# Kernel tuning notes

Hardware: AMD Instinct MI355X
Metric: run time of the kernel (lower is better)

## Reference

```python
import jax, jax.numpy as jnp
import numpy as np

N_NODES = 100000
NUM_LAYER = 3
REG_WEIGHT = 1e-4


def setup_inputs() -> dict:
    key = jax.random.key(0)
    ks = jax.random.split(key, 6)
    E = 1280000
    B = 4096
    D = 64
    # xavier-uniform-like scale for embedding table
    emb_weight = jax.random.normal(ks[0], (N_NODES, D), dtype=jnp.float32) * 0.01
    src = jax.random.randint(ks[1], (E,), 0, N_NODES, dtype=jnp.int32)
    dst = jax.random.randint(ks[2], (E,), 0, N_NODES, dtype=jnp.int32)
    users = jax.random.randint(ks[3], (B,), 0, N_NODES, dtype=jnp.int32)
    pos = jax.random.randint(ks[4], (B,), 0, N_NODES, dtype=jnp.int32)
    neg = jax.random.randint(ks[5], (B,), 0, N_NODES, dtype=jnp.int32)
    return {"emb_weight": emb_weight, "src": src, "dst": dst,
            "users": users, "pos": pos, "neg": neg}


def _edge_norm(src, dst):
    # DGL norm(): d = sum of edge mask (ones) per dst node; adj_e = d[src]^-0.5 * d[dst]^-0.5
    ones = jnp.ones(src.shape[0], dtype=jnp.float32)
    deg = jax.ops.segment_sum(ones, dst, num_segments=N_NODES)
    dinv = jnp.where(deg > 0, deg ** -0.5, 0.0)  # inf -> 0 handling
    return dinv[src] * dinv[dst]  # [E]


def _propagate(emb_weight, src, dst, adj):
    # LightGCN propagation: h_{l+1}[v] = sum_{(u->v)} adj_e * h_l[u]
    h = emb_weight
    layers = [h]
    for _ in range(NUM_LAYER):
        m = h[src] * adj[:, None]                    # [E, D] gather + edge weight
        h = jax.ops.segment_sum(m, dst, num_segments=N_NODES)  # [N, D] scatter-sum
        layers.append(h)
    return jnp.mean(jnp.stack(layers, axis=1), axis=1)  # mean over L+1 layers


def reference(emb_weight, src, dst, users, pos, neg):
    adj = _edge_norm(src, dst)
    all_emb = _propagate(emb_weight, src, dst, adj)

    u_e, p_e, n_e = all_emb[users], all_emb[pos], all_emb[neg]
    u0, p0, n0 = emb_weight[users], emb_weight[pos], emb_weight[neg]

    B = users.shape[0]
    reg_loss = 0.5 * (jnp.sum(u0 ** 2) + jnp.sum(p0 ** 2) + jnp.sum(n0 ** 2)) / B
    reg_loss = reg_loss * REG_WEIGHT

    pos_scores = jnp.sum(u_e * p_e, axis=1)
    neg_scores = jnp.sum(u_e * n_e, axis=1)
    loss_emb = jnp.mean(jax.nn.softplus(neg_scores - pos_scores))

    loss = loss_emb + reg_loss
    return loss, loss_emb, reg_loss
```

## Files before the change

### kernel.cpp

```cpp
#include <hip/hip_runtime.h>
#include <hip/hip_fp8.h>
#include <math.h>

#define N_NODES 100000
#define DIM 64
#define NUM_LAYER 3
#define BATCH 4096
#define REG_WEIGHT 1e-4f
#define NBUCKET 391
#define STAGE_CAP 4096
#define CURPAD 16
#define H_SCALE 64.0f
#define H_INV_SCALE (1.0f / 64.0f)

typedef float floatx2 __attribute__((ext_vector_type(2)));

__device__ unsigned char g_hf8[2][(size_t)N_NODES * DIM];
__device__ float g_sums[(size_t)3 * BATCH * DIM];
__device__ int   g_row_ptr[N_NODES + 1];
__device__ float g_dinv[N_NODES];
__device__ int   g_bcur[NBUCKET * CURPAD];
__device__ unsigned int g_stage[NBUCKET * STAGE_CAP];
__device__ int   g_csr[1280000];
__device__ int2  g_csr2[1280000];
__device__ int   g_shead[N_NODES];
__device__ int   g_snext[3 * BATCH];
__device__ float g_part_sp[BATCH];
__device__ float g_part_rg[BATCH];

__device__ inline void fma4_fp8(unsigned int d, float w,
                                float& a0, float& a1, float& a2, float& a3) {
    floatx2 lo = __builtin_amdgcn_cvt_pk_f32_fp8((int)d, false);
    floatx2 hi = __builtin_amdgcn_cvt_pk_f32_fp8((int)d, true);
    a0 = fmaf(w, lo.x, a0); a1 = fmaf(w, lo.y, a1);
    a2 = fmaf(w, hi.x, a2); a3 = fmaf(w, hi.y, a3);
}
__device__ inline unsigned int pack4_fp8(float a0, float a1, float a2, float a3) {
    int w = __builtin_amdgcn_cvt_pk_fp8_f32(a0, a1, 0, false);
    w     = __builtin_amdgcn_cvt_pk_fp8_f32(a2, a3, w, true);
    return (unsigned int)w;
}

#define EDGES_PER_THREAD 8
__global__ void __launch_bounds__(1024) stage_buckets(const int* __restrict__ src,
                                                      const int* __restrict__ dst, int E,
                                                      const int* __restrict__ users,
                                                      const int* __restrict__ pos,
                                                      const int* __restrict__ neg,
                                                      const float* __restrict__ emb) {
    __shared__ int h[NBUCKET];
    __shared__ int cur[NBUCKET];
    int tid = threadIdx.x;
    int gt = blockIdx.x * 1024 + tid;
    if (gt < 3 * BATCH) {
        int which = gt / BATCH, s = gt - which * BATCH;
        const int* idx = (which == 0) ? users : ((which == 1) ? pos : neg);
        g_snext[gt] = atomicExch(&g_shead[idx[s]], gt + 1);
    }
    int base = blockIdx.x * (1024 * EDGES_PER_THREAD);
    for (int i = tid; i < NBUCKET; i += 1024) h[i] = 0;
    __syncthreads();
    int myd[EDGES_PER_THREAD], mys[EDGES_PER_THREAD];
    #pragma unroll
    for (int k = 0; k < EDGES_PER_THREAD; ++k) {
        int e = base + k * 1024 + tid;
        if (e < E) {
            myd[k] = dst[e]; mys[k] = src[e];
            atomicAdd(&h[myd[k] >> 8], 1);
        } else myd[k] = -1;
    }
    __syncthreads();
    for (int i = tid; i < NBUCKET; i += 1024) {
        int c = h[i];
        cur[i] = c ? (atomicAdd(&g_bcur[i * CURPAD], c) + i * STAGE_CAP) : 0;
    }
    __syncthreads();
    #pragma unroll
    for (int k = 0; k < EDGES_PER_THREAD; ++k) {
        if (myd[k] >= 0) {
            int p = atomicAdd(&cur[myd[k] >> 8], 1);
            g_stage[p] = (unsigned int)((mys[k] << 8) | (myd[k] & 255));
        }
    }
    {
        const int NW = N_NODES * DIM / 4;
        int stride = gridDim.x * 1024;
        unsigned int* hw = (unsigned int*)g_hf8[0];
        for (int k = blockIdx.x * 1024 + tid; k < NW; k += stride) {
            const float* e = emb + (size_t)k * 4;
            hw[k] = pack4_fp8(e[0] * H_SCALE, e[1] * H_SCALE,
                              e[2] * H_SCALE, e[3] * H_SCALE);
        }
    }
}

__global__ void __launch_bounds__(512) finalize_place() {
    __shared__ int cs[512];
    __shared__ int lh[256], sc[256], cur[256];
    int b = blockIdx.x, t = threadIdx.x;
    int c = (t < NBUCKET) ? g_bcur[t * CURPAD] : 0;
    cs[t] = c;
    __syncthreads();
    for (int off = 1; off < 512; off <<= 1) {
        int x = (t >= off) ? cs[t - off] : 0;
        __syncthreads();
        cs[t] += x;
        __syncthreads();
    }
    int mybase = (b > 0) ? cs[b - 1] : 0;
    int cnt    = cs[b] - mybase;
    if (b == 0 && t == 0) g_row_ptr[N_NODES] = cs[NBUCKET - 1];
    int sbeg = b * STAGE_CAP;
    if (t < 256) lh[t] = 0;
    __syncthreads();
    for (int k = t; k < cnt; k += 512)
        atomicAdd(&lh[g_stage[sbeg + k] & 255], 1);
    __syncthreads();
    int v = 0;
    if (t < 256) { v = lh[t]; sc[t] = v; }
    __syncthreads();
    for (int off = 1; off < 256; off <<= 1) {
        int x = (t >= off && t < 256) ? sc[t - off] : 0;
        __syncthreads();
        if (t < 256) sc[t] += x;
        __syncthreads();
    }
    if (t < 256) {
        int start = mybase + sc[t] - v;
        cur[t] = start;
        int node = (b << 8) + t;
        if (node < N_NODES) {
            g_row_ptr[node] = start;
            g_dinv[node]    = (v > 0) ? rsqrtf((float)v) : 0.0f;
        }
    }
    __syncthreads();
    for (int k = t; k < cnt; k += 512) {
        unsigned int e = g_stage[sbeg + k];
        int pos = atomicAdd(&cur[e & 255], 1);
        g_csr[pos] = (int)(e >> 8);
    }
}

__global__ void build_wcsr(int E) {
    int i = blockIdx.x * blockDim.x + threadIdx.x;
    if (i < E) {
        int s = g_csr[i];
        g_csr2[i] = make_int2(s, __float_as_int(g_dinv[s]));
    }
}

__global__ void pull_layer_fp8(const unsigned char* __restrict__ h,
                               unsigned char* __restrict__ hn, int do_gather) {
    int gid0 = blockIdx.x * blockDim.x + threadIdx.x;
    if (do_gather && gid0 < NBUCKET) g_bcur[gid0 * CURPAD] = 0;
    int wid  = gid0 >> 6;
    int lane = threadIdx.x & 63;
    int g  = lane >> 4;
    int li = lane & 15;
    int n = wid * 4 + g;
    if (n >= N_NODES) return;
    int beg = g_row_ptr[n], end = g_row_ptr[n + 1];
    float dinvN = g_dinv[n];
    float a0 = 0.f, a1 = 0.f, a2 = 0.f, a3 = 0.f;
    for (int k = beg; k < end; k += 4) {
        int k1 = min(k + 1, end - 1);
        int k2 = min(k + 2, end - 1);
        int k3 = min(k + 3, end - 1);
        int2 e0 = g_csr2[k];
        int2 e1 = g_csr2[k1];
        int2 e2 = g_csr2[k2];
        int2 e3 = g_csr2[k3];
        unsigned int d0 = *(const unsigned int*)(h + (size_t)e0.x * DIM + li * 4);
        unsigned int d1 = *(const unsigned int*)(h + (size_t)e1.x * DIM + li * 4);
        unsigned int d2 = *(const unsigned int*)(h + (size_t)e2.x * DIM + li * 4);
        unsigned int d3 = *(const unsigned int*)(h + (size_t)e3.x * DIM + li * 4);
        float w0 = __int_as_float(e0.y) * dinvN;
        float w1 = (k + 1 < end) ? __int_as_float(e1.y) * dinvN : 0.0f;
        float w2 = (k + 2 < end) ? __int_as_float(e2.y) * dinvN : 0.0f;
        float w3 = (k + 3 < end) ? __int_as_float(e3.y) * dinvN : 0.0f;
        fma4_fp8(d0, w0, a0, a1, a2, a3);
        fma4_fp8(d1, w1, a0, a1, a2, a3);
        fma4_fp8(d2, w2, a0, a1, a2, a3);
        fma4_fp8(d3, w3, a0, a1, a2, a3);
    }
    *(unsigned int*)(hn + (size_t)n * DIM + li * 4) = pack4_fp8(a0, a1, a2, a3);
    if (do_gather) {
        int sidx = g_shead[n];
        while (sidx > 0) {
            int sr = sidx - 1;
            float* sp = &g_sums[(size_t)sr * DIM + li * 4];
            sp[0] = a0 * H_INV_SCALE; sp[1] = a1 * H_INV_SCALE;
            sp[2] = a2 * H_INV_SCALE; sp[3] = a3 * H_INV_SCALE;
            sidx = g_snext[sr];
        }
        if (li == 0) g_shead[n] = 0;
    }
}

__global__ void pull_sampled(const unsigned char* __restrict__ h,
                             const int* __restrict__ users, const int* __restrict__ pos,
                             const int* __restrict__ neg) {
    int gid0 = blockIdx.x * blockDim.x + threadIdx.x;
    int wid  = gid0 >> 6;
    int lane = threadIdx.x & 63;
    int g  = lane >> 4;
    int li = lane & 15;
    int s = wid * 4 + g;
    if (s >= 3 * BATCH) return;
    int which = s >> 12;
    int i     = s & (BATCH - 1);
    const int* idx = (which == 0) ? users : ((which == 1) ? pos : neg);
    int node = idx[i];
    int beg = g_row_ptr[node], end = g_row_ptr[node + 1];
    float dinvN = g_dinv[node];
    float a0 = 0.f, a1 = 0.f, a2 = 0.f, a3 = 0.f;
    for (int k = beg; k < end; k += 4) {
        int k1 = min(k + 1, end - 1);
        int k2 = min(k + 2, end - 1);
        int k3 = min(k + 3, end - 1);
        int2 e0 = g_csr2[k];
        int2 e1 = g_csr2[k1];
        int2 e2 = g_csr2[k2];
        int2 e3 = g_csr2[k3];
        unsigned int d0 = *(const unsigned int*)(h + (size_t)e0.x * DIM + li * 4);
        unsigned int d1 = *(const unsigned int*)(h + (size_t)e1.x * DIM + li * 4);
        unsigned int d2 = *(const unsigned int*)(h + (size_t)e2.x * DIM + li * 4);
        unsigned int d3 = *(const unsigned int*)(h + (size_t)e3.x * DIM + li * 4);
        float w0 = __int_as_float(e0.y) * dinvN;
        float w1 = (k + 1 < end) ? __int_as_float(e1.y) * dinvN : 0.0f;
        float w2 = (k + 2 < end) ? __int_as_float(e2.y) * dinvN : 0.0f;
        float w3 = (k + 3 < end) ? __int_as_float(e3.y) * dinvN : 0.0f;
        fma4_fp8(d0, w0, a0, a1, a2, a3);
        fma4_fp8(d1, w1, a0, a1, a2, a3);
        fma4_fp8(d2, w2, a0, a1, a2, a3);
        fma4_fp8(d3, w3, a0, a1, a2, a3);
    }
    unsigned int dn = *(const unsigned int*)(h + (size_t)node * DIM + li * 4);
    floatx2 lo = __builtin_amdgcn_cvt_pk_f32_fp8((int)dn, false);
    floatx2 hi = __builtin_amdgcn_cvt_pk_f32_fp8((int)dn, true);
    float* sp = &g_sums[(size_t)s * DIM + li * 4];
    sp[0] += (a0 + lo.x) * H_INV_SCALE;
    sp[1] += (a1 + lo.y) * H_INV_SCALE;
    sp[2] += (a2 + hi.x) * H_INV_SCALE;
    sp[3] += (a3 + hi.y) * H_INV_SCALE;
}

__global__ void score_reduce(const float* __restrict__ emb,
                             const int* __restrict__ users, const int* __restrict__ pos,
                             const int* __restrict__ neg) {
    int wid  = (blockIdx.x * blockDim.x + threadIdx.x) >> 6;
    int lane = threadIdx.x & 63;
    if (wid >= BATCH) return;
    float u0 = emb[(size_t)users[wid] * DIM + lane];
    float p0 = emb[(size_t)pos[wid]   * DIM + lane];
    float n0 = emb[(size_t)neg[wid]   * DIM + lane];
    float u = 0.25f * (g_sums[(size_t)wid * DIM + lane] + u0);
    float p = 0.25f * (g_sums[(size_t)(BATCH + wid) * DIM + lane] + p0);
    float n = 0.25f * (g_sums[(size_t)(2 * BATCH + wid) * DIM + lane] + n0);
    float ps = u * p;
    float ns = u * n;
    float rg = u0 * u0 + p0 * p0 + n0 * n0;
    #pragma unroll
    for (int off = 32; off > 0; off >>= 1) {
        ps += __shfl_down(ps, off);
        ns += __shfl_down(ns, off);
        rg += __shfl_down(rg, off);
    }
    if (lane == 0) {
        float x  = ns - ps;
        float sp = fmaxf(x, 0.0f) + log1pf(expf(-fabsf(x)));
        g_part_sp[wid] = sp;
        g_part_rg[wid] = rg;
    }
}

__global__ void final_reduce(float* __restrict__ out) {
    __shared__ float s_sp[256], s_rg[256];
    int t = threadIdx.x;
    float sp = 0.0f, rg = 0.0f;
    for (int i = t; i < BATCH; i += 256) { sp += g_part_sp[i]; rg += g_part_rg[i]; }
    s_sp[t] = sp; s_rg[t] = rg;
    __syncthreads();
    for (int off = 128; off > 0; off >>= 1) {
        if (t < off) { s_sp[t] += s_sp[t + off]; s_rg[t] += s_rg[t + off]; }
        __syncthreads();
    }
    if (t == 0) {
        float loss_emb = s_sp[0] / (float)BATCH;
        float reg      = 0.5f * s_rg[0] / (float)BATCH * REG_WEIGHT;
        out[0] = loss_emb + reg;
        out[1] = loss_emb;
        out[2] = reg;
    }
}

extern "C" void kernel_launch(void* const* d_in, const int* in_sizes, int n_in,
                              void* d_out, int out_size, void* d_ws, size_t ws_size,
                              hipStream_t stream) {
    const float* emb   = (const float*)d_in[0];
    const int*   src   = (const int*)d_in[1];
    const int*   dst   = (const int*)d_in[2];
    const int*   users = (const int*)d_in[3];
    const int*   pos   = (const int*)d_in[4];
    const int*   neg   = (const int*)d_in[5];
    const int E = in_sizes[1];
    float* out = (float*)d_out;

    unsigned char* hf_a;  hipGetSymbolAddress((void**)&hf_a, HIP_SYMBOL(g_hf8));
    unsigned char* hf_b = hf_a + (size_t)N_NODES * DIM;

    const int STAGE_BLOCKS = (E + 1024 * EDGES_PER_THREAD - 1) / (1024 * EDGES_PER_THREAD);
    stage_buckets<<<STAGE_BLOCKS, 1024, 0, stream>>>(src, dst, E, users, pos, neg, emb);
    finalize_place<<<NBUCKET, 512, 0, stream>>>();
    build_wcsr<<<(E + 255) / 256, 256, 0, stream>>>(E);

    const int NQUAD = (N_NODES + 3) / 4;
    const int PULL_BLOCKS = (NQUAD * 64 + 255) / 256;

    pull_layer_fp8<<<PULL_BLOCKS, 256, 0, stream>>>(hf_a, hf_b, 1);

    pull_layer_fp8<<<PULL_BLOCKS, 256, 0, stream>>>(hf_b, hf_a, 0);

    const int SAMP_BLOCKS = ((3 * BATCH + 3) / 4 * 64 + 255) / 256;
    pull_sampled<<<SAMP_BLOCKS, 256, 0, stream>>>(hf_a, users, pos, neg);

    score_reduce<<<(BATCH * 64 + 255) / 256, 256, 0, stream>>>(emb, users, pos, neg);
    final_reduce<<<1, 256, 0, stream>>>(out);
}
```

Before: 187.4 us.

## Fold symmetric degree normalization into node scaling and drop weighted CSR build

Each propagated table now stores h scaled by dinv, so edge weights become one and only the plain source index is read per edge. This removes the build_wcsr kernel and halves per-edge index traffic. The fp8 conversion of the embedding moves into finalize_place, so it can apply the per-node dinv, and the second layer now accumulates sampled rows, so pull_sampled no longer re-reads the self row. The fp8 scale rises to 256 to keep precision in the pre-scaled values, which raises the risk of overflow or precision loss. Edges per thread in staging also drop from 8 to 4.

```diff
diff --git a/kernel.cpp b/kernel.cpp
--- a/kernel.cpp
+++ b/kernel.cpp
@@ -10,8 +10,8 @@
 #define NBUCKET 391
 #define STAGE_CAP 4096
 #define CURPAD 16
-#define H_SCALE 64.0f
-#define H_INV_SCALE (1.0f / 64.0f)
+#define H_SCALE 256.0f
+#define H_INV_SCALE (1.0f / 256.0f)
 
 typedef float floatx2 __attribute__((ext_vector_type(2)));
 
@@ -22,7 +22,6 @@
 __device__ int   g_bcur[NBUCKET * CURPAD];
 __device__ unsigned int g_stage[NBUCKET * STAGE_CAP];
 __device__ int   g_csr[1280000];
-__device__ int2  g_csr2[1280000];
 __device__ int   g_shead[N_NODES];
 __device__ int   g_snext[3 * BATCH];
 __device__ float g_part_sp[BATCH];
@@ -41,13 +40,12 @@
     return (unsigned int)w;
 }
 
-#define EDGES_PER_THREAD 8
+#define EDGES_PER_THREAD 4
 __global__ void __launch_bounds__(1024) stage_buckets(const int* __restrict__ src,
                                                       const int* __restrict__ dst, int E,
                                                       const int* __restrict__ users,
                                                       const int* __restrict__ pos,
-                                                      const int* __restrict__ neg,
-                                                      const float* __restrict__ emb) {
+                                                      const int* __restrict__ neg) {
     __shared__ int h[NBUCKET];
     __shared__ int cur[NBUCKET];
     int tid = threadIdx.x;
@@ -82,21 +80,12 @@
             g_stage[p] = (unsigned int)((mys[k] << 8) | (myd[k] & 255));
         }
     }
-    {
-        const int NW = N_NODES * DIM / 4;
-        int stride = gridDim.x * 1024;
-        unsigned int* hw = (unsigned int*)g_hf8[0];
-        for (int k = blockIdx.x * 1024 + tid; k < NW; k += stride) {
-            const float* e = emb + (size_t)k * 4;
-            hw[k] = pack4_fp8(e[0] * H_SCALE, e[1] * H_SCALE,
-                              e[2] * H_SCALE, e[3] * H_SCALE);
-        }
-    }
-}
-
-__global__ void __launch_bounds__(512) finalize_place() {
+}
+
+__global__ void __launch_bounds__(512) finalize_place(const float* __restrict__ emb) {
     __shared__ int cs[512];
     __shared__ int lh[256], sc[256], cur[256];
+    __shared__ float ldv[256];
     int b = blockIdx.x, t = threadIdx.x;
     int c = (t < NBUCKET) ? g_bcur[t * CURPAD] : 0;
     cs[t] = c;
@@ -128,10 +117,12 @@
     if (t < 256) {
         int start = mybase + sc[t] - v;
         cur[t] = start;
+        float dv = (v > 0) ? rsqrtf((float)v) : 0.0f;
+        ldv[t] = dv;
         int node = (b << 8) + t;
         if (node < N_NODES) {
             g_row_ptr[node] = start;
-            g_dinv[node]    = (v > 0) ? rsqrtf((float)v) : 0.0f;
+            g_dinv[node]    = dv;
         }
     }
     __syncthreads();
@@ -140,20 +131,24 @@
         int pos = atomicAdd(&cur[e & 255], 1);
         g_csr[pos] = (int)(e >> 8);
     }
-}
-
-__global__ void build_wcsr(int E) {
-    int i = blockIdx.x * blockDim.x + threadIdx.x;
-    if (i < E) {
-        int s = g_csr[i];
-        g_csr2[i] = make_int2(s, __float_as_int(g_dinv[s]));
+    {
+        int nbase = b << 8;
+        int rows = N_NODES - nbase; if (rows > 256) rows = 256;
+        unsigned int* hw = (unsigned int*)g_hf8[0];
+        for (int idx = t; idx < rows * 16; idx += 512) {
+            int row = idx >> 4, li = idx & 15;
+            const float4 ev = *(const float4*)(emb + (size_t)(nbase + row) * DIM + li * 4);
+            float s = ldv[row] * H_SCALE;
+            hw[(size_t)(nbase + row) * 16 + li] =
+                pack4_fp8(ev.x * s, ev.y * s, ev.z * s, ev.w * s);
+        }
     }
 }
 
 __global__ void pull_layer_fp8(const unsigned char* __restrict__ h,
-                               unsigned char* __restrict__ hn, int do_gather) {
+                               unsigned char* __restrict__ hn, int mode) {
     int gid0 = blockIdx.x * blockDim.x + threadIdx.x;
-    if (do_gather && gid0 < NBUCKET) g_bcur[gid0 * CURPAD] = 0;
+    if (mode == 1 && gid0 < NBUCKET) g_bcur[gid0 * CURPAD] = 0;
     int wid  = gid0 >> 6;
     int lane = threadIdx.x & 63;
     int g  = lane >> 4;
@@ -167,34 +162,41 @@
         int k1 = min(k + 1, end - 1);
         int k2 = min(k + 2, end - 1);
         int k3 = min(k + 3, end - 1);
-        int2 e0 = g_csr2[k];
-        int2 e1 = g_csr2[k1];
-        int2 e2 = g_csr2[k2];
-        int2 e3 = g_csr2[k3];
-        unsigned int d0 = *(const unsigned int*)(h + (size_t)e0.x * DIM + li * 4);
-        unsigned int d1 = *(const unsigned int*)(h + (size_t)e1.x * DIM + li * 4);
-        unsigned int d2 = *(const unsigned int*)(h + (size_t)e2.x * DIM + li * 4);
-        unsigned int d3 = *(const unsigned int*)(h + (size_t)e3.x * DIM + li * 4);
-        float w0 = __int_as_float(e0.y) * dinvN;
-        float w1 = (k + 1 < end) ? __int_as_float(e1.y) * dinvN : 0.0f;
-        float w2 = (k + 2 < end) ? __int_as_float(e2.y) * dinvN : 0.0f;
-        float w3 = (k + 3 < end) ? __int_as_float(e3.y) * dinvN : 0.0f;
-        fma4_fp8(d0, w0, a0, a1, a2, a3);
+        int s0 = g_csr[k];
+        int s1 = g_csr[k1];
+        int s2 = g_csr[k2];
+        int s3 = g_csr[k3];
+        unsigned int d0 = *(const unsigned int*)(h + (size_t)s0 * DIM + li * 4);
+        unsigned int d1 = *(const unsigned int*)(h + (size_t)s1 * DIM + li * 4);
+        unsigned int d2 = *(const unsigned int*)(h + (size_t)s2 * DIM + li * 4);
+        unsigned int d3 = *(const unsigned int*)(h + (size_t)s3 * DIM + li * 4);
+        float w1 = (k + 1 < end) ? 1.0f : 0.0f;
+        float w2 = (k + 2 < end) ? 1.0f : 0.0f;
+        float w3 = (k + 3 < end) ? 1.0f : 0.0f;
+        fma4_fp8(d0, 1.0f, a0, a1, a2, a3);
         fma4_fp8(d1, w1, a0, a1, a2, a3);
         fma4_fp8(d2, w2, a0, a1, a2, a3);
         fma4_fp8(d3, w3, a0, a1, a2, a3);
     }
-    *(unsigned int*)(hn + (size_t)n * DIM + li * 4) = pack4_fp8(a0, a1, a2, a3);
-    if (do_gather) {
+    float dd = dinvN * dinvN;
+    *(unsigned int*)(hn + (size_t)n * DIM + li * 4) =
+        pack4_fp8(a0 * dd, a1 * dd, a2 * dd, a3 * dd);
+    if (mode) {
+        float gw = dinvN * H_INV_SCALE;
         int sidx = g_shead[n];
         while (sidx > 0) {
             int sr = sidx - 1;
             float* sp = &g_sums[(size_t)sr * DIM + li * 4];
-            sp[0] = a0 * H_INV_SCALE; sp[1] = a1 * H_INV_SCALE;
-            sp[2] = a2 * H_INV_SCALE; sp[3] = a3 * H_INV_SCALE;
+            if (mode == 1) {
+                sp[0] = a0 * gw; sp[1] = a1 * gw;
+                sp[2] = a2 * gw; sp[3] = a3 * gw;
+            } else {
+                sp[0] += a0 * gw; sp[1] += a1 * gw;
+                sp[2] += a2 * gw; sp[3] += a3 * gw;
+            }
             sidx = g_snext[sr];
         }
-        if (li == 0) g_shead[n] = 0;
+        if (mode == 2 && li == 0) g_shead[n] = 0;
     }
 }
 
@@ -219,31 +221,28 @@
         int k1 = min(k + 1, end - 1);
         int k2 = min(k + 2, end - 1);
         int k3 = min(k + 3, end - 1);
-        int2 e0 = g_csr2[k];
-        int2 e1 = g_csr2[k1];
-        int2 e2 = g_csr2[k2];
-        int2 e3 = g_csr2[k3];
-        unsigned int d0 = *(const unsigned int*)(h + (size_t)e0.x * DIM + li * 4);
-        unsigned int d1 = *(const unsigned int*)(h + (size_t)e1.x * DIM + li * 4);
-        unsigned int d2 = *(const unsigned int*)(h + (size_t)e2.x * DIM + li * 4);
-        unsigned int d3 = *(const unsigned int*)(h + (size_t)e3.x * DIM + li * 4);
-        float w0 = __int_as_float(e0.y) * dinvN;
-        float w1 = (k + 1 < end) ? __int_as_float(e1.y) * dinvN : 0.0f;
-        float w2 = (k + 2 < end) ? __int_as_float(e2.y) * dinvN : 0.0f;
-        float w3 = (k + 3 < end) ? __int_as_float(e3.y) * dinvN : 0.0f;
-        fma4_fp8(d0, w0, a0, a1, a2, a3);
+        int s0 = g_csr[k];
+        int s1 = g_csr[k1];
+        int s2 = g_csr[k2];
+        int s3 = g_csr[k3];
+        unsigned int d0 = *(const unsigned int*)(h + (size_t)s0 * DIM + li * 4);
+        unsigned int d1 = *(const unsigned int*)(h + (size_t)s1 * DIM + li * 4);
+        unsigned int d2 = *(const unsigned int*)(h + (size_t)s2 * DIM + li * 4);
+        unsigned int d3 = *(const unsigned int*)(h + (size_t)s3 * DIM + li * 4);
+        float w1 = (k + 1 < end) ? 1.0f : 0.0f;
+        float w2 = (k + 2 < end) ? 1.0f : 0.0f;
+        float w3 = (k + 3 < end) ? 1.0f : 0.0f;
+        fma4_fp8(d0, 1.0f, a0, a1, a2, a3);
         fma4_fp8(d1, w1, a0, a1, a2, a3);
         fma4_fp8(d2, w2, a0, a1, a2, a3);
         fma4_fp8(d3, w3, a0, a1, a2, a3);
     }
-    unsigned int dn = *(const unsigned int*)(h + (size_t)node * DIM + li * 4);
-    floatx2 lo = __builtin_amdgcn_cvt_pk_f32_fp8((int)dn, false);
-    floatx2 hi = __builtin_amdgcn_cvt_pk_f32_fp8((int)dn, true);
+    float gw = dinvN * H_INV_SCALE;
     float* sp = &g_sums[(size_t)s * DIM + li * 4];
-    sp[0] += (a0 + lo.x) * H_INV_SCALE;
-    sp[1] += (a1 + lo.y) * H_INV_SCALE;
-    sp[2] += (a2 + hi.x) * H_INV_SCALE;
-    sp[3] += (a3 + hi.y) * H_INV_SCALE;
+    sp[0] += a0 * gw;
+    sp[1] += a1 * gw;
+    sp[2] += a2 * gw;
+    sp[3] += a3 * gw;
 }
 
 __global__ void score_reduce(const float* __restrict__ emb,
@@ -311,16 +310,15 @@
     unsigned char* hf_b = hf_a + (size_t)N_NODES * DIM;
 
     const int STAGE_BLOCKS = (E + 1024 * EDGES_PER_THREAD - 1) / (1024 * EDGES_PER_THREAD);
-    stage_buckets<<<STAGE_BLOCKS, 1024, 0, stream>>>(src, dst, E, users, pos, neg, emb);
-    finalize_place<<<NBUCKET, 512, 0, stream>>>();
-    build_wcsr<<<(E + 255) / 256, 256, 0, stream>>>(E);
+    stage_buckets<<<STAGE_BLOCKS, 1024, 0, stream>>>(src, dst, E, users, pos, neg);
+    finalize_place<<<NBUCKET, 512, 0, stream>>>(emb);
 
     const int NQUAD = (N_NODES + 3) / 4;
     const int PULL_BLOCKS = (NQUAD * 64 + 255) / 256;
 
     pull_layer_fp8<<<PULL_BLOCKS, 256, 0, stream>>>(hf_a, hf_b, 1);
 
-    pull_layer_fp8<<<PULL_BLOCKS, 256, 0, stream>>>(hf_b, hf_a, 0);
+    pull_layer_fp8<<<PULL_BLOCKS, 256, 0, stream>>>(hf_b, hf_a, 2);
 
     const int SAMP_BLOCKS = ((3 * BATCH + 3) / 4 * 64 + 255) / 256;
     pull_sampled<<<SAMP_BLOCKS, 256, 0, stream>>>(hf_a, users, pos, neg);
```

Measured after the change: 185.4 us. Within noise of the previous version (-1.1%).
